# Kernel optimization log

Hardware: AMD Instinct MI355X
Metric: run time of the kernel (lower is better)

## Reference

```python
import jax, jax.numpy as jnp
import numpy as np

EMBED_DIM = 768
NUM_HEADS = 12
HEAD_DIM = EMBED_DIM // NUM_HEADS
B, S = 2, 2048


def setup_inputs() -> dict:
    key = jax.random.key(0)
    ks = jax.random.split(key, 6)
    glorot = jnp.sqrt(6.0 / (EMBED_DIM + EMBED_DIM)).astype(jnp.float32)
    x = jax.random.normal(ks[0], (B, S, EMBED_DIM), dtype=jnp.float32)
    mask = jnp.zeros((1, 1, S, S), dtype=jnp.float32)  # additive mask, 0 = no masking
    Wq = jax.random.uniform(ks[1], (EMBED_DIM, EMBED_DIM), jnp.float32, -glorot, glorot)
    Wk = jax.random.uniform(ks[2], (EMBED_DIM, EMBED_DIM), jnp.float32, -glorot, glorot)
    Wv = jax.random.uniform(ks[3], (EMBED_DIM, EMBED_DIM), jnp.float32, -glorot, glorot)
    Wo = jax.random.uniform(ks[4], (EMBED_DIM, EMBED_DIM), jnp.float32, -glorot, glorot)
    bo = jnp.zeros((EMBED_DIM,), dtype=jnp.float32)
    return {"x": x, "mask": mask, "Wq": Wq, "Wk": Wk, "Wv": Wv, "Wo": Wo, "bo": bo}


def reference(x, mask, Wq, Wk, Wv, Wo, bo):
    b, s, _ = x.shape
    # Q/K/V projections (no bias), split into heads: [b, h, s, d]
    def split_heads(t):
        return t.reshape(b, s, NUM_HEADS, HEAD_DIM).transpose(0, 2, 1, 3)
    q = split_heads(x @ Wq)
    k = split_heads(x @ Wk)
    v = split_heads(x @ Wv)
    scale = 1.0 / jnp.sqrt(jnp.float32(HEAD_DIM))
    logits = jnp.einsum('bhqd,bhkd->bhqk', q, k) * scale  # [b, h, s, s]
    logits = logits + mask * (-1e9)
    weights = jax.nn.softmax(logits, axis=-1)
    attn = jnp.einsum('bhqk,bhkd->bhqd', weights, v)
    concat = attn.transpose(0, 2, 1, 3).reshape(b, s, EMBED_DIM)
    return concat @ Wo + bo
```

## Files before the change

### kernel.cpp

```cpp
#include <hip/hip_runtime.h>


typedef __bf16 bf16_t;
typedef bf16_t bf16x8 __attribute__((ext_vector_type(8)));
typedef bf16_t bf16x4 __attribute__((ext_vector_type(4)));
typedef float f32x4 __attribute__((ext_vector_type(4)));
typedef _Float16 f16x4 __attribute__((ext_vector_type(4)));
typedef __fp16 hf2 __attribute__((ext_vector_type(2)));

#define SC2 0.1803368801111137f

__device__ __forceinline__ float bf2f(unsigned short u) {
  union { unsigned int i; float f; } x;
  x.i = ((unsigned int)u) << 16;
  return x.f;
}

__device__ __forceinline__ float fexp2(float x) {
  return __builtin_amdgcn_exp2f(x);
}

__device__ __forceinline__ void glds16(const bf16_t* g, bf16_t* l) {
  __builtin_amdgcn_global_load_lds(
      (const __attribute__((address_space(1))) void*)g,
      (__attribute__((address_space(3))) void*)l, 16, 0, 0);
}

__device__ __forceinline__ int detect_bf16_flag(const unsigned short* x) {
  const int lane = threadIdx.x & 63;
  const uint4* p = (const uint4*)x;
  uint4 a = p[lane * 2];
  uint4 b = p[lane * 2 + 1];
  unsigned int w[8] = {a.x, a.y, a.z, a.w, b.x, b.y, b.z, b.w};
  unsigned int big = 0;
#pragma unroll
  for (int i = 0; i < 8; i++) {
    unsigned int e0 = (w[i] >> 7) & 0xFF, e1 = (w[i] >> 23) & 0xFF;
    big |= (e0 > 0x88u) | (e1 > 0x88u);
  }
  unsigned long long bal = __ballot(big != 0u);
  return bal == 0ULL ? 1 : 0;
}

__global__ void k_prep(const void* __restrict__ x, const void* __restrict__ mask,
                       const void* __restrict__ Wq, const void* __restrict__ Wk,
                       const void* __restrict__ Wv, const void* __restrict__ Wo,
                       bf16_t* __restrict__ xb, bf16_t* __restrict__ wqkvT,
                       bf16_t* __restrict__ woT, int* __restrict__ mflags) {
  __shared__ float ts[32][33];
  __shared__ int snz;
  const int blk = blockIdx.x;
  const int f = detect_bf16_flag((const unsigned short*)x);

  if (blk < 1536) {
    if (f) return;
    int i = blk * 256 + threadIdx.x;
    const float* xf = (const float*)x + (size_t)i * 8;
    bf16x8 v;
#pragma unroll
    for (int j = 0; j < 8; j++) v[j] = (bf16_t)xf[j];
    *(bf16x8*)(xb + (size_t)i * 8) = v;
  } else if (blk < 3840) {
    const int t = blk - 1536;
    const int z = t / 576, r = t % 576, kt = r / 24, nt = r % 24;
    const void* wsrc = (z == 0) ? Wq : (z == 1) ? Wk : (z == 2) ? Wv : Wo;
    bf16_t* dst = (z < 3) ? (wqkvT + (size_t)z * 768 * 768) : woT;
    const int c = threadIdx.x & 31, r0 = threadIdx.x >> 5;
#pragma unroll
    for (int i = 0; i < 4; i++) {
      int kr = kt * 32 + r0 + i * 8;
      float v;
      if (f) v = bf2f(((const unsigned short*)wsrc)[(size_t)kr * 768 + nt * 32 + c]);
      else   v = ((const float*)wsrc)[(size_t)kr * 768 + nt * 32 + c];
      ts[r0 + i * 8][c] = v;
    }
    __syncthreads();
#pragma unroll
    for (int i = 0; i < 4; i++) {
      int nr = nt * 32 + r0 + i * 8;
      dst[(size_t)nr * 768 + kt * 32 + c] = (bf16_t)ts[c][r0 + i * 8];
    }
  } else {
    const int t = blk - 3840;
    const int qt = t >> 4, ktm = t & 15;
    if (threadIdx.x == 0) snz = 0;
    __syncthreads();
    unsigned int nz = 0;
    if (f) {
#pragma unroll
      for (int i = 0; i < 8; i++) {
        int uidx = i * 256 + threadIdx.x;
        int row = uidx >> 4, col = uidx & 15;
        const uint4* p = (const uint4*)((const char*)mask +
            ((size_t)(qt * 128 + row) * 2048 + ktm * 128) * 2 + col * 16);
        uint4 v = *p;
        nz |= ((v.x | v.y | v.z | v.w) & 0x7fff7fffu);
      }
    } else {
#pragma unroll
      for (int i = 0; i < 16; i++) {
        int uidx = i * 256 + threadIdx.x;
        int row = uidx >> 5, col = uidx & 31;
        const uint4* p = (const uint4*)((const char*)mask +
            ((size_t)(qt * 128 + row) * 2048 + ktm * 128) * 4 + col * 16);
        uint4 v = *p;
        nz |= ((v.x | v.y | v.z | v.w) & 0x7fffffffu);
      }
    }
    if (nz) snz = 1;
    __syncthreads();
    if (threadIdx.x == 0) mflags[qt * 16 + ktm] = snz;
  }
}

__global__ __launch_bounds__(256, 3) void k_gemmQKV(
    const bf16_t* __restrict__ xb, const bf16_t* __restrict__ Bm,
    bf16_t* __restrict__ Qd, bf16_t* __restrict__ Kd, _Float16* __restrict__ Vt,
    const unsigned short* __restrict__ xdet) {
  __shared__ __align__(16) char smem[32768];
  bf16_t* As0 = (bf16_t*)smem;
  bf16_t* As1 = (bf16_t*)(smem + 8192);
  bf16_t* Bs0 = (bf16_t*)(smem + 16384);
  bf16_t* Bs1 = (bf16_t*)(smem + 24576);
  _Float16* Tb = (_Float16*)smem;

  const int f = detect_bf16_flag(xdet);
  const bf16_t* A = f ? (const bf16_t*)xdet : xb;

  const int tid = threadIdx.x;
  const int n0 = blockIdx.x * 128, m0 = blockIdx.y * 128;
  const int r = tid >> 2, c8 = (tid & 3) << 3;
  const bf16_t* Ag = A + (size_t)(m0 + r) * 768 + c8;
  const bf16_t* Bg = Bm + (size_t)(n0 + r) * 768 + c8;
  const int wid = tid >> 6, lane = tid & 63;
  const int wm = (wid >> 1) << 6, wn = (wid & 1) << 6;
  const int lr = lane & 15, lk = (lane >> 4) << 3, g4 = (lane >> 4) << 2;

  f32x4 acc[4][4];
  const f32x4 z = {0.f, 0.f, 0.f, 0.f};
#pragma unroll
  for (int i = 0; i < 4; i++)
#pragma unroll
    for (int j = 0; j < 4; j++) acc[i][j] = z;

  for (int k0 = 0; k0 < 768; k0 += 64) {
    glds16(Ag + k0, As0 + wid * 512);
    glds16(Ag + (size_t)64 * 768 + k0, As0 + 2048 + wid * 512);
    glds16(Ag + k0 + 32, As1 + wid * 512);
    glds16(Ag + (size_t)64 * 768 + k0 + 32, As1 + 2048 + wid * 512);
    glds16(Bg + k0, Bs0 + wid * 512);
    glds16(Bg + (size_t)64 * 768 + k0, Bs0 + 2048 + wid * 512);
    glds16(Bg + k0 + 32, Bs1 + wid * 512);
    glds16(Bg + (size_t)64 * 768 + k0 + 32, Bs1 + 2048 + wid * 512);
    __syncthreads();
#pragma unroll
    for (int kc = 0; kc < 2; kc++) {
      const bf16_t* Asb = kc ? As1 : As0;
      const bf16_t* Bsb = kc ? Bs1 : Bs0;
      bf16x8 af[4], bf_[4];
#pragma unroll
      for (int t = 0; t < 4; t++) af[t]  = *(const bf16x8*)&Asb[(wm + t * 16 + lr) * 32 + lk];
#pragma unroll
      for (int t = 0; t < 4; t++) bf_[t] = *(const bf16x8*)&Bsb[(wn + t * 16 + lr) * 32 + lk];
#pragma unroll
      for (int i = 0; i < 4; i++)
#pragma unroll
        for (int j = 0; j < 4; j++)
          acc[i][j] = __builtin_amdgcn_mfma_f32_16x16x32_bf16(af[i], bf_[j], acc[i][j], 0, 0, 0);
    }
    __syncthreads();
  }

  if (n0 < 1536) {
    bf16_t* dst = (n0 < 768) ? Qd : Kd;
    const int nb = (n0 < 768) ? n0 : n0 - 768;
    const int bb = m0 >> 11;
#pragma unroll
    for (int i = 0; i < 4; i++)
#pragma unroll
      for (int j = 0; j < 4; j++) {
        const int rc = nb + wn + j * 16 + lr;
        const int hh = rc >> 6, dd = rc & 63;
        const size_t base = (((size_t)bb * 12 + hh) * 2048) * 64 + dd;
#pragma unroll
        for (int reg = 0; reg < 4; reg++) {
          const int s = (m0 & 2047) + wm + i * 16 + g4 + reg;
          dst[base + (size_t)s * 64] = (bf16_t)acc[i][j][reg];
        }
      }
  } else {
    const int bb = m0 >> 11;
#pragma unroll
    for (int half = 0; half < 2; half++) {
      if ((wid & 1) == half) {
#pragma unroll
        for (int j = 0; j < 4; j++) {
          const int d_l = j * 16 + lr;
#pragma unroll
          for (int i = 0; i < 4; i++)
#pragma unroll
            for (int reg = 0; reg < 4; reg++)
              Tb[d_l * 136 + wm + i * 16 + g4 + reg] = (_Float16)acc[i][j][reg];
        }
      }
      __syncthreads();
      const int row = tid >> 2, cc = (tid & 3) * 32;
      const int vcol = (n0 - 1536) + half * 64 + row;
      const int hh = vcol >> 6;
      _Float16* dstv = Vt + (((size_t)bb * 12 + hh) * 64 + row) * 2048 + (m0 & 2047) + cc;
#pragma unroll
      for (int u = 0; u < 4; u++)
        *(uint4*)(dstv + u * 8) = *(const uint4*)&Tb[row * 136 + cc + u * 8];
      __syncthreads();
    }
  }
}

__global__ __launch_bounds__(320, 4) void k_flash(
    const bf16_t* __restrict__ Qd, const bf16_t* __restrict__ Kd,
    const _Float16* __restrict__ Vt, const void* __restrict__ mask,
    const int* __restrict__ mflags, const unsigned short* __restrict__ xdet,
    bf16_t* __restrict__ attn) {
  __shared__ __align__(16) char sm[32768];

  const int tid = threadIdx.x, wid = tid >> 6, lane = tid & 63;
  const int lr = lane & 15, quad = lane >> 4, lk = quad << 3, g4 = quad << 2;

  const int lin = blockIdx.x;
  const int gx = lin & 7, ww = lin >> 3;
  const int hb = gx * 3 + (ww >> 5);
  const int h = hb % 12, bb = hb / 12;
  const int qt = ww & 31;

  const size_t bh = (size_t)bb * 12 + h;
  const char* Kh = (const char*)(Kd + bh * 2048 * 64);
  const char* Vh = (const char*)(Vt + bh * 64 * 2048);

  if (wid == 4) {
    const char* kS[8]; const char* vS[8];
#pragma unroll
    for (int u = 0; u < 8; u++) {
      const int R = (u >> 1) * 16 + lr;
      const int c = (u & 1) * 4 + quad;
      kS[u] = Kh + R * 128 + c * 16;
      const int u2 = u * 2 + (lane >> 5);
      const int dtv = u2 & 3, ctv = u2 >> 2, j2 = lane & 31;
      vS[u] = Vh + (size_t)(dtv * 16 + (j2 & 15)) * 4096 + ctv * 32 + (j2 >> 4) * 16;
    }
    uint4 kv[8], vv[8];
#pragma unroll
    for (int u = 0; u < 8; u++) kv[u] = *(const uint4*)(kS[u]);
#pragma unroll
    for (int u = 0; u < 8; u++) vv[u] = *(const uint4*)(vS[u]);
#pragma unroll
    for (int u = 0; u < 8; u++) *(uint4*)(sm + u * 1024 + lane * 16) = kv[u];
#pragma unroll
    for (int u = 0; u < 8; u++) *(uint4*)(sm + 8192 + u * 1024 + lane * 16) = vv[u];
    __syncthreads();
    for (int s = 0; s < 32; s++) {
      if (s < 31) {
        const int t = s + 1;
        char* buf = sm + (t & 1) * 16384;
#pragma unroll
        for (int u = 0; u < 8; u++) kv[u] = *(const uint4*)(kS[u] + (size_t)t * 8192);
#pragma unroll
        for (int u = 0; u < 8; u++) vv[u] = *(const uint4*)(vS[u] + (size_t)t * 128);
#pragma unroll
        for (int u = 0; u < 8; u++) *(uint4*)(buf + u * 1024 + lane * 16) = kv[u];
#pragma unroll
        for (int u = 0; u < 8; u++) *(uint4*)(buf + 8192 + u * 1024 + lane * 16) = vv[u];
      }
      __syncthreads();
    }
    return;
  }

  const bf16_t* Qh = Qd + bh * 2048 * 64;
  const int q0 = qt * 64 + wid * 16;
  const int mbf = detect_bf16_flag(xdet);
  const int* mfrow = mflags + (qt >> 1) * 16;
  int mbits = 0;
#pragma unroll
  for (int t = 0; t < 16; t++) mbits |= (mfrow[t] != 0) << t;

  const bf16x8 qf0 = *(const bf16x8*)&Qh[(size_t)(q0 + lr) * 64 + lk];
  const bf16x8 qf1 = *(const bf16x8*)&Qh[(size_t)(q0 + lr) * 64 + 32 + lk];

  f16x4 ones;
  ones[0] = (_Float16)1.f; ones[1] = (_Float16)1.f;
  ones[2] = (_Float16)1.f; ones[3] = (_Float16)1.f;

  const f32x4 z = {0.f, 0.f, 0.f, 0.f};
  f32x4 ot[4];
#pragma unroll
  for (int dt = 0; dt < 4; dt++) ot[dt] = z;
  float mrow = -1e30f, lrow = 0.f;

  __syncthreads();

  for (int s = 0; s < 32; s++) {
    const char* Kc = sm + (s & 1) * 16384;
    const char* Vc = Kc + 8192;

    f32x4 sv[4];
#pragma unroll
    for (int ct = 0; ct < 4; ct++) sv[ct] = z;
#pragma unroll
    for (int ct = 0; ct < 4; ct++) {
      bf16x8 kf0 = *(const bf16x8*)(Kc + ct * 2048 + lane * 16);
      bf16x8 kf1 = *(const bf16x8*)(Kc + ct * 2048 + 1024 + lane * 16);
      sv[ct] = __builtin_amdgcn_mfma_f32_16x16x32_bf16(kf0, qf0, sv[ct], 0, 0, 0);
      sv[ct] = __builtin_amdgcn_mfma_f32_16x16x32_bf16(kf1, qf1, sv[ct], 0, 0, 0);
    }

    if ((mbits >> (s >> 1)) & 1) {
#pragma unroll
      for (int ct = 0; ct < 4; ct++)
#pragma unroll
        for (int reg = 0; reg < 4; reg++) {
          size_t mi = (size_t)(q0 + lr) * 2048 + s * 64 + ct * 16 + g4 + reg;
          float mv = mbf ? bf2f(((const unsigned short*)mask)[mi])
                         : ((const float*)mask)[mi];
          sv[ct][reg] -= 8e9f * mv;
        }
    }

    float t = fmaxf(
        fmaxf(fmaxf(fmaxf(sv[0][0], sv[0][1]), fmaxf(sv[0][2], sv[0][3])),
              fmaxf(fmaxf(sv[1][0], sv[1][1]), fmaxf(sv[1][2], sv[1][3]))),
        fmaxf(fmaxf(fmaxf(sv[2][0], sv[2][1]), fmaxf(sv[2][2], sv[2][3])),
              fmaxf(fmaxf(sv[3][0], sv[3][1]), fmaxf(sv[3][2], sv[3][3]))));
    t = fmaxf(t, __shfl_xor(t, 16));
    t = fmaxf(t, __shfl_xor(t, 32));
    const float mnew = fmaxf(mrow, t);
    if (__ballot(mnew > mrow)) {
      const float alpha = fexp2((mrow - mnew) * SC2);
#pragma unroll
      for (int dt = 0; dt < 4; dt++)
#pragma unroll
        for (int reg = 0; reg < 4; reg++) ot[dt][reg] *= alpha;
      lrow *= alpha;
    }
    mrow = mnew;
    const float mS = mnew * SC2;

    f16x4 pb[4];
#pragma unroll
    for (int ct = 0; ct < 4; ct++) {
      float p0 = fexp2(fmaf(sv[ct][0], SC2, -mS));
      float p1 = fexp2(fmaf(sv[ct][1], SC2, -mS));
      float p2 = fexp2(fmaf(sv[ct][2], SC2, -mS));
      float p3 = fexp2(fmaf(sv[ct][3], SC2, -mS));
      union { hf2 h[2]; f16x4 v; } u;
      u.h[0] = __builtin_amdgcn_cvt_pkrtz(p0, p1);
      u.h[1] = __builtin_amdgcn_cvt_pkrtz(p2, p3);
      pb[ct] = u.v;
    }

    f32x4 asum = z;
#pragma unroll
    for (int ct = 0; ct < 4; ct++) {
      asum = __builtin_amdgcn_mfma_f32_16x16x16f16(ones, pb[ct], asum, 0, 0, 0);
#pragma unroll
      for (int dt = 0; dt < 4; dt++) {
        f16x4 va = *(const f16x4*)(Vc + (ct * 4 + dt) * 512 +
                                   (quad >> 1) * 256 + lr * 16 + (quad & 1) * 8);
        ot[dt] = __builtin_amdgcn_mfma_f32_16x16x16f16(va, pb[ct], ot[dt], 0, 0, 0);
      }
    }
    lrow += asum[0];
    __syncthreads();
  }

  const float inv = 1.0f / lrow;
  bf16_t* arow = attn + ((size_t)bb * 2048 + q0 + lr) * 768 + h * 64 + g4;
#pragma unroll
  for (int dt = 0; dt < 4; dt++) {
    bf16x4 v;
#pragma unroll
    for (int reg = 0; reg < 4; reg++) v[reg] = (bf16_t)(ot[dt][reg] * inv);
    *(bf16x4*)(arow + dt * 16) = v;
  }
}

__global__ __launch_bounds__(256, 3) void k_gemm2(
    const bf16_t* __restrict__ A, const bf16_t* __restrict__ Bm,
    const void* __restrict__ bo, const unsigned short* __restrict__ xdet,
    float* __restrict__ outF, unsigned short* __restrict__ outH) {
  __shared__ __align__(16) char smem[16384];
  bf16_t* As0 = (bf16_t*)smem;
  bf16_t* As1 = (bf16_t*)(smem + 4096);
  bf16_t* Bs0 = (bf16_t*)(smem + 8192);
  bf16_t* Bs1 = (bf16_t*)(smem + 12288);

  const int tid = threadIdx.x, wid = tid >> 6, lane = tid & 63;
  const int n0 = blockIdx.x * 64, m0 = blockIdx.y * 64;
  const int wm = (wid >> 1) << 5, wn = (wid & 1) << 5;
  const int lr = lane & 15, lk = (lane >> 4) << 3, g4 = (lane >> 4) << 2;
  const int rr = lane >> 2, c8 = (lane & 3) << 3;
  const bf16_t* Ag = A + (size_t)(m0 + wid * 16 + rr) * 768 + c8;
  const bf16_t* Bg = Bm + (size_t)(n0 + wid * 16 + rr) * 768 + c8;

  f32x4 acc[2][2];
  const f32x4 z = {0.f, 0.f, 0.f, 0.f};
#pragma unroll
  for (int i = 0; i < 2; i++)
#pragma unroll
    for (int j = 0; j < 2; j++) acc[i][j] = z;

  for (int k0 = 0; k0 < 768; k0 += 64) {
    glds16(Ag + k0, As0 + wid * 512);
    glds16(Ag + k0 + 32, As1 + wid * 512);
    glds16(Bg + k0, Bs0 + wid * 512);
    glds16(Bg + k0 + 32, Bs1 + wid * 512);
    __syncthreads();
#pragma unroll
    for (int kc = 0; kc < 2; kc++) {
      const bf16_t* Asb = kc ? As1 : As0;
      const bf16_t* Bsb = kc ? Bs1 : Bs0;
      bf16x8 af[2], bf_[2];
#pragma unroll
      for (int i = 0; i < 2; i++) af[i]  = *(const bf16x8*)&Asb[(wm + i * 16 + lr) * 32 + lk];
#pragma unroll
      for (int j = 0; j < 2; j++) bf_[j] = *(const bf16x8*)&Bsb[(wn + j * 16 + lr) * 32 + lk];
#pragma unroll
      for (int i = 0; i < 2; i++)
#pragma unroll
        for (int j = 0; j < 2; j++)
          acc[i][j] = __builtin_amdgcn_mfma_f32_16x16x32_bf16(af[i], bf_[j], acc[i][j], 0, 0, 0);
    }
    __syncthreads();
  }

  const int obf = detect_bf16_flag(xdet);
#pragma unroll
  for (int i = 0; i < 2; i++)
#pragma unroll
    for (int j = 0; j < 2; j++) {
      const int nn = n0 + wn + j * 16 + lr;
      const float bv = obf ? bf2f(((const unsigned short*)bo)[nn])
                           : ((const float*)bo)[nn];
#pragma unroll
      for (int reg = 0; reg < 4; reg++) {
        const int m = m0 + wm + i * 16 + g4 + reg;
        const float v = acc[i][j][reg] + bv;
        if (obf) outH[(size_t)m * 768 + nn] = __builtin_bit_cast(unsigned short, (bf16_t)v);
        else     outF[(size_t)m * 768 + nn] = v;
      }
    }
}

extern "C" void kernel_launch(void* const* d_in, const int* in_sizes, int n_in,
                              void* d_out, int out_size, void* d_ws, size_t ws_size,
                              hipStream_t stream) {
  (void)in_sizes; (void)n_in; (void)out_size; (void)ws_size;
  const void* x    = d_in[0];
  const void* mask = d_in[1];
  const void* Wq   = d_in[2];
  const void* Wk   = d_in[3];
  const void* Wv   = d_in[4];
  const void* Wo   = d_in[5];
  const void* bo   = d_in[6];

  char* w = (char*)d_ws;
  size_t off = 0;
  auto take = [&](size_t b) -> void* {
    void* p = w + off;
    off = (off + b + 255) & ~(size_t)255;
    return p;
  };
  int*      mflags = (int*)take(256 * 4);
  bf16_t*   wqkvT  = (bf16_t*)take((size_t)2304 * 768 * 2);
  bf16_t*   woT    = (bf16_t*)take((size_t)768 * 768 * 2);
  bf16_t*   xb     = (bf16_t*)take((size_t)4096 * 768 * 2);
  bf16_t*   Qd     = (bf16_t*)take((size_t)3145728 * 2);
  bf16_t*   Kd     = (bf16_t*)take((size_t)3145728 * 2);
  _Float16* Vt     = (_Float16*)take((size_t)3145728 * 2);
  bf16_t*   attn   = xb;

  k_prep<<<4096, 256, 0, stream>>>(x, mask, Wq, Wk, Wv, Wo, xb, wqkvT, woT, mflags);
  k_gemmQKV<<<dim3(18, 32), 256, 0, stream>>>(xb, wqkvT, Qd, Kd, Vt,
                                              (const unsigned short*)x);
  k_flash<<<768, 320, 0, stream>>>(Qd, Kd, Vt, mask, mflags,
                                   (const unsigned short*)x, attn);
  k_gemm2<<<dim3(12, 64), 256, 0, stream>>>(attn, woT, bo, (const unsigned short*)x,
                                            (float*)d_out, (unsigned short*)d_out);
}
```

Baseline: 182.0 us.

## Add dedicated producer wave for double-buffered loads in projection GEMMs

Both GEMM kernels now launch 320 threads, and a fifth wave acts as a producer. It loads A/B tiles from global memory through registers into a double-buffered LDS ring, one K-step ahead, while the four compute waves run MFMAs on the other buffer. This replaces the synchronous global_load_lds pattern, where every wave loaded and then waited each iteration, and is meant to overlap memory latency with compute. The cost is more barriers (24 K-steps of 32 instead of 12 of 64) and a serial single-wave load path that may be bandwidth-limited. The producer wave must also match barrier counts in the QKV epilogue.

```diff
diff --git a/kernel.cpp b/kernel.cpp
--- a/kernel.cpp
+++ b/kernel.cpp
@@ -18,12 +18,6 @@
 
 __device__ __forceinline__ float fexp2(float x) {
   return __builtin_amdgcn_exp2f(x);
-}
-
-__device__ __forceinline__ void glds16(const bf16_t* g, bf16_t* l) {
-  __builtin_amdgcn_global_load_lds(
-      (const __attribute__((address_space(1))) void*)g,
-      (__attribute__((address_space(3))) void*)l, 16, 0, 0);
 }
 
 __device__ __forceinline__ int detect_bf16_flag(const unsigned short* x) {
@@ -113,29 +107,58 @@
   }
 }
 
-__global__ __launch_bounds__(256, 3) void k_gemmQKV(
+__global__ __launch_bounds__(320, 4) void k_gemmQKV(
     const bf16_t* __restrict__ xb, const bf16_t* __restrict__ Bm,
     bf16_t* __restrict__ Qd, bf16_t* __restrict__ Kd, _Float16* __restrict__ Vt,
     const unsigned short* __restrict__ xdet) {
   __shared__ __align__(16) char smem[32768];
-  bf16_t* As0 = (bf16_t*)smem;
-  bf16_t* As1 = (bf16_t*)(smem + 8192);
-  bf16_t* Bs0 = (bf16_t*)(smem + 16384);
-  bf16_t* Bs1 = (bf16_t*)(smem + 24576);
   _Float16* Tb = (_Float16*)smem;
 
   const int f = detect_bf16_flag(xdet);
   const bf16_t* A = f ? (const bf16_t*)xdet : xb;
 
-  const int tid = threadIdx.x;
+  const int tid = threadIdx.x, wid = tid >> 6, lane = tid & 63;
   const int n0 = blockIdx.x * 128, m0 = blockIdx.y * 128;
-  const int r = tid >> 2, c8 = (tid & 3) << 3;
-  const bf16_t* Ag = A + (size_t)(m0 + r) * 768 + c8;
-  const bf16_t* Bg = Bm + (size_t)(n0 + r) * 768 + c8;
-  const int wid = tid >> 6, lane = tid & 63;
+  const int lr = lane & 15, lk = (lane >> 4) << 3, g4 = (lane >> 4) << 2;
+
+  if (wid == 4) {
+    const int pr = lane >> 2, pk = (lane & 3) << 3;
+    const bf16_t* Ag = A + (size_t)(m0 + pr) * 768 + pk;
+    const bf16_t* Bg = Bm + (size_t)(n0 + pr) * 768 + pk;
+    const int dst16 = lane * 16;
+    uint4 av[8], bv[8];
+#pragma unroll
+    for (int j = 0; j < 8; j++) av[j] = *(const uint4*)(Ag + (size_t)(j * 16) * 768);
+#pragma unroll
+    for (int j = 0; j < 8; j++) bv[j] = *(const uint4*)(Bg + (size_t)(j * 16) * 768);
+#pragma unroll
+    for (int j = 0; j < 8; j++) *(uint4*)(smem + j * 1024 + dst16) = av[j];
+#pragma unroll
+    for (int j = 0; j < 8; j++) *(uint4*)(smem + 16384 + j * 1024 + dst16) = bv[j];
+    __syncthreads();
+    for (int s = 0; s < 24; s++) {
+      if (s < 23) {
+        const int k0 = (s + 1) * 32;
+        char* Ab = smem + ((s + 1) & 1) * 8192;
+        char* Bb = smem + 16384 + ((s + 1) & 1) * 8192;
+#pragma unroll
+        for (int j = 0; j < 8; j++) av[j] = *(const uint4*)(Ag + (size_t)(j * 16) * 768 + k0);
+#pragma unroll
+        for (int j = 0; j < 8; j++) bv[j] = *(const uint4*)(Bg + (size_t)(j * 16) * 768 + k0);
+#pragma unroll
+        for (int j = 0; j < 8; j++) *(uint4*)(Ab + j * 1024 + dst16) = av[j];
+#pragma unroll
+        for (int j = 0; j < 8; j++) *(uint4*)(Bb + j * 1024 + dst16) = bv[j];
+      }
+      __syncthreads();
+    }
+    if (n0 < 1536) return;
+#pragma unroll
+    for (int half = 0; half < 2; half++) { __syncthreads(); __syncthreads(); }
+    return;
+  }
+
   const int wm = (wid >> 1) << 6, wn = (wid & 1) << 6;
-  const int lr = lane & 15, lk = (lane >> 4) << 3, g4 = (lane >> 4) << 2;
-
   f32x4 acc[4][4];
   const f32x4 z = {0.f, 0.f, 0.f, 0.f};
 #pragma unroll
@@ -143,31 +166,20 @@
 #pragma unroll
     for (int j = 0; j < 4; j++) acc[i][j] = z;
 
-  for (int k0 = 0; k0 < 768; k0 += 64) {
-    glds16(Ag + k0, As0 + wid * 512);
-    glds16(Ag + (size_t)64 * 768 + k0, As0 + 2048 + wid * 512);
-    glds16(Ag + k0 + 32, As1 + wid * 512);
-    glds16(Ag + (size_t)64 * 768 + k0 + 32, As1 + 2048 + wid * 512);
-    glds16(Bg + k0, Bs0 + wid * 512);
-    glds16(Bg + (size_t)64 * 768 + k0, Bs0 + 2048 + wid * 512);
-    glds16(Bg + k0 + 32, Bs1 + wid * 512);
-    glds16(Bg + (size_t)64 * 768 + k0 + 32, Bs1 + 2048 + wid * 512);
-    __syncthreads();
-#pragma unroll
-    for (int kc = 0; kc < 2; kc++) {
-      const bf16_t* Asb = kc ? As1 : As0;
-      const bf16_t* Bsb = kc ? Bs1 : Bs0;
-      bf16x8 af[4], bf_[4];
-#pragma unroll
-      for (int t = 0; t < 4; t++) af[t]  = *(const bf16x8*)&Asb[(wm + t * 16 + lr) * 32 + lk];
-#pragma unroll
-      for (int t = 0; t < 4; t++) bf_[t] = *(const bf16x8*)&Bsb[(wn + t * 16 + lr) * 32 + lk];
-#pragma unroll
-      for (int i = 0; i < 4; i++)
-#pragma unroll
-        for (int j = 0; j < 4; j++)
-          acc[i][j] = __builtin_amdgcn_mfma_f32_16x16x32_bf16(af[i], bf_[j], acc[i][j], 0, 0, 0);
-    }
+  __syncthreads();
+  for (int s = 0; s < 24; s++) {
+    const bf16_t* As = (const bf16_t*)(smem + (s & 1) * 8192);
+    const bf16_t* Bs = (const bf16_t*)(smem + 16384 + (s & 1) * 8192);
+    bf16x8 af[4], bf_[4];
+#pragma unroll
+    for (int t = 0; t < 4; t++) af[t]  = *(const bf16x8*)&As[(wm + t * 16 + lr) * 32 + lk];
+#pragma unroll
+    for (int t = 0; t < 4; t++) bf_[t] = *(const bf16x8*)&Bs[(wn + t * 16 + lr) * 32 + lk];
+#pragma unroll
+    for (int i = 0; i < 4; i++)
+#pragma unroll
+      for (int j = 0; j < 4; j++)
+        acc[i][j] = __builtin_amdgcn_mfma_f32_16x16x32_bf16(af[i], bf_[j], acc[i][j], 0, 0, 0);
     __syncthreads();
   }
 
@@ -383,24 +395,51 @@
   }
 }
 
-__global__ __launch_bounds__(256, 3) void k_gemm2(
+__global__ __launch_bounds__(320, 4) void k_gemm2(
     const bf16_t* __restrict__ A, const bf16_t* __restrict__ Bm,
     const void* __restrict__ bo, const unsigned short* __restrict__ xdet,
     float* __restrict__ outF, unsigned short* __restrict__ outH) {
   __shared__ __align__(16) char smem[16384];
-  bf16_t* As0 = (bf16_t*)smem;
-  bf16_t* As1 = (bf16_t*)(smem + 4096);
-  bf16_t* Bs0 = (bf16_t*)(smem + 8192);
-  bf16_t* Bs1 = (bf16_t*)(smem + 12288);
 
   const int tid = threadIdx.x, wid = tid >> 6, lane = tid & 63;
   const int n0 = blockIdx.x * 64, m0 = blockIdx.y * 64;
+  const int lr = lane & 15, lk = (lane >> 4) << 3, g4 = (lane >> 4) << 2;
+
+  if (wid == 4) {
+    const int pr = lane >> 2, pk = (lane & 3) << 3;
+    const bf16_t* Ag = A + (size_t)(m0 + pr) * 768 + pk;
+    const bf16_t* Bg = Bm + (size_t)(n0 + pr) * 768 + pk;
+    const int dst16 = lane * 16;
+    uint4 av[4], bv[4];
+#pragma unroll
+    for (int j = 0; j < 4; j++) av[j] = *(const uint4*)(Ag + (size_t)(j * 16) * 768);
+#pragma unroll
+    for (int j = 0; j < 4; j++) bv[j] = *(const uint4*)(Bg + (size_t)(j * 16) * 768);
+#pragma unroll
+    for (int j = 0; j < 4; j++) *(uint4*)(smem + j * 1024 + dst16) = av[j];
+#pragma unroll
+    for (int j = 0; j < 4; j++) *(uint4*)(smem + 8192 + j * 1024 + dst16) = bv[j];
+    __syncthreads();
+    for (int s = 0; s < 24; s++) {
+      if (s < 23) {
+        const int k0 = (s + 1) * 32;
+        char* Ab = smem + ((s + 1) & 1) * 4096;
+        char* Bb = smem + 8192 + ((s + 1) & 1) * 4096;
+#pragma unroll
+        for (int j = 0; j < 4; j++) av[j] = *(const uint4*)(Ag + (size_t)(j * 16) * 768 + k0);
+#pragma unroll
+        for (int j = 0; j < 4; j++) bv[j] = *(const uint4*)(Bg + (size_t)(j * 16) * 768 + k0);
+#pragma unroll
+        for (int j = 0; j < 4; j++) *(uint4*)(Ab + j * 1024 + dst16) = av[j];
+#pragma unroll
+        for (int j = 0; j < 4; j++) *(uint4*)(Bb + j * 1024 + dst16) = bv[j];
+      }
+      __syncthreads();
+    }
+    return;
+  }
+
   const int wm = (wid >> 1) << 5, wn = (wid & 1) << 5;
-  const int lr = lane & 15, lk = (lane >> 4) << 3, g4 = (lane >> 4) << 2;
-  const int rr = lane >> 2, c8 = (lane & 3) << 3;
-  const bf16_t* Ag = A + (size_t)(m0 + wid * 16 + rr) * 768 + c8;
-  const bf16_t* Bg = Bm + (size_t)(n0 + wid * 16 + rr) * 768 + c8;
-
   f32x4 acc[2][2];
   const f32x4 z = {0.f, 0.f, 0.f, 0.f};
 #pragma unroll
@@ -408,27 +447,20 @@
 #pragma unroll
     for (int j = 0; j < 2; j++) acc[i][j] = z;
 
-  for (int k0 = 0; k0 < 768; k0 += 64) {
-    glds16(Ag + k0, As0 + wid * 512);
-    glds16(Ag + k0 + 32, As1 + wid * 512);
-    glds16(Bg + k0, Bs0 + wid * 512);
-    glds16(Bg + k0 + 32, Bs1 + wid * 512);
-    __syncthreads();
-#pragma unroll
-    for (int kc = 0; kc < 2; kc++) {
-      const bf16_t* Asb = kc ? As1 : As0;
-      const bf16_t* Bsb = kc ? Bs1 : Bs0;
-      bf16x8 af[2], bf_[2];
-#pragma unroll
-      for (int i = 0; i < 2; i++) af[i]  = *(const bf16x8*)&Asb[(wm + i * 16 + lr) * 32 + lk];
-#pragma unroll
-      for (int j = 0; j < 2; j++) bf_[j] = *(const bf16x8*)&Bsb[(wn + j * 16 + lr) * 32 + lk];
-#pragma unroll
-      for (int i = 0; i < 2; i++)
-#pragma unroll
-        for (int j = 0; j < 2; j++)
-          acc[i][j] = __builtin_amdgcn_mfma_f32_16x16x32_bf16(af[i], bf_[j], acc[i][j], 0, 0, 0);
-    }
+  __syncthreads();
+  for (int s = 0; s < 24; s++) {
+    const bf16_t* As = (const bf16_t*)(smem + (s & 1) * 4096);
+    const bf16_t* Bs = (const bf16_t*)(smem + 8192 + (s & 1) * 4096);
+    bf16x8 af[2], bf_[2];
+#pragma unroll
+    for (int i = 0; i < 2; i++) af[i]  = *(const bf16x8*)&As[(wm + i * 16 + lr) * 32 + lk];
+#pragma unroll
+    for (int j = 0; j < 2; j++) bf_[j] = *(const bf16x8*)&Bs[(wn + j * 16 + lr) * 32 + lk];
+#pragma unroll
+    for (int i = 0; i < 2; i++)
+#pragma unroll
+      for (int j = 0; j < 2; j++)
+        acc[i][j] = __builtin_amdgcn_mfma_f32_16x16x32_bf16(af[i], bf_[j], acc[i][j], 0, 0, 0);
     __syncthreads();
   }
 
@@ -479,10 +511,10 @@
   bf16_t*   attn   = xb;
 
   k_prep<<<4096, 256, 0, stream>>>(x, mask, Wq, Wk, Wv, Wo, xb, wqkvT, woT, mflags);
-  k_gemmQKV<<<dim3(18, 32), 256, 0, stream>>>(xb, wqkvT, Qd, Kd, Vt,
+  k_gemmQKV<<<dim3(18, 32), 320, 0, stream>>>(xb, wqkvT, Qd, Kd, Vt,
                                               (const unsigned short*)x);
   k_flash<<<768, 320, 0, stream>>>(Qd, Kd, Vt, mask, mflags,
                                    (const unsigned short*)x, attn);
-  k_gemm2<<<dim3(12, 64), 256, 0, stream>>>(attn, woT, bo, (const unsigned short*)x,
+  k_gemm2<<<dim3(12, 64), 320, 0, stream>>>(attn, woT, bo, (const unsigned short*)x,
                                             (float*)d_out, (unsigned short*)d_out);
 }
```

Measured after the change: 192.3 us. 1.06x slower.

## Double-buffer LDS tiles in QKV and output projection GEMMs

Applied to the files above, without the earlier changes.

Both projection GEMM kernels now use double-buffered shared memory. The next k-slice is prefetched through global_load_lds while MFMAs run on the current buffer, with one barrier per step instead of two. The aim is to hide global load latency behind compute. The QKV kernel now steps by a k-depth of 32 (24 steps), and the output kernel's LDS grows to 32KB, which may reduce occupancy.

```diff
diff --git a/kernel.cpp b/kernel.cpp
--- a/kernel.cpp
+++ b/kernel.cpp
@@ -118,10 +118,6 @@
     bf16_t* __restrict__ Qd, bf16_t* __restrict__ Kd, _Float16* __restrict__ Vt,
     const unsigned short* __restrict__ xdet) {
   __shared__ __align__(16) char smem[32768];
-  bf16_t* As0 = (bf16_t*)smem;
-  bf16_t* As1 = (bf16_t*)(smem + 8192);
-  bf16_t* Bs0 = (bf16_t*)(smem + 16384);
-  bf16_t* Bs1 = (bf16_t*)(smem + 24576);
   _Float16* Tb = (_Float16*)smem;
 
   const int f = detect_bf16_flag(xdet);
@@ -143,31 +139,38 @@
 #pragma unroll
     for (int j = 0; j < 4; j++) acc[i][j] = z;
 
-  for (int k0 = 0; k0 < 768; k0 += 64) {
-    glds16(Ag + k0, As0 + wid * 512);
-    glds16(Ag + (size_t)64 * 768 + k0, As0 + 2048 + wid * 512);
-    glds16(Ag + k0 + 32, As1 + wid * 512);
-    glds16(Ag + (size_t)64 * 768 + k0 + 32, As1 + 2048 + wid * 512);
-    glds16(Bg + k0, Bs0 + wid * 512);
-    glds16(Bg + (size_t)64 * 768 + k0, Bs0 + 2048 + wid * 512);
-    glds16(Bg + k0 + 32, Bs1 + wid * 512);
-    glds16(Bg + (size_t)64 * 768 + k0 + 32, Bs1 + 2048 + wid * 512);
-    __syncthreads();
-#pragma unroll
-    for (int kc = 0; kc < 2; kc++) {
-      const bf16_t* Asb = kc ? As1 : As0;
-      const bf16_t* Bsb = kc ? Bs1 : Bs0;
-      bf16x8 af[4], bf_[4];
-#pragma unroll
-      for (int t = 0; t < 4; t++) af[t]  = *(const bf16x8*)&Asb[(wm + t * 16 + lr) * 32 + lk];
-#pragma unroll
-      for (int t = 0; t < 4; t++) bf_[t] = *(const bf16x8*)&Bsb[(wn + t * 16 + lr) * 32 + lk];
-#pragma unroll
-      for (int i = 0; i < 4; i++)
-#pragma unroll
-        for (int j = 0; j < 4; j++)
-          acc[i][j] = __builtin_amdgcn_mfma_f32_16x16x32_bf16(af[i], bf_[j], acc[i][j], 0, 0, 0);
-    }
+  {
+    bf16_t* A0 = (bf16_t*)smem;
+    bf16_t* B0 = (bf16_t*)(smem + 16384);
+    glds16(Ag, A0 + wid * 512);
+    glds16(Ag + (size_t)64 * 768, A0 + 2048 + wid * 512);
+    glds16(Bg, B0 + wid * 512);
+    glds16(Bg + (size_t)64 * 768, B0 + 2048 + wid * 512);
+  }
+  __syncthreads();
+
+  for (int s = 0; s < 24; s++) {
+    if (s < 23) {
+      const int k0 = (s + 1) * 32;
+      bf16_t* An = (bf16_t*)(smem + ((s + 1) & 1) * 8192);
+      bf16_t* Bn = (bf16_t*)(smem + 16384 + ((s + 1) & 1) * 8192);
+      glds16(Ag + k0, An + wid * 512);
+      glds16(Ag + (size_t)64 * 768 + k0, An + 2048 + wid * 512);
+      glds16(Bg + k0, Bn + wid * 512);
+      glds16(Bg + (size_t)64 * 768 + k0, Bn + 2048 + wid * 512);
+    }
+    const bf16_t* As = (const bf16_t*)(smem + (s & 1) * 8192);
+    const bf16_t* Bs = (const bf16_t*)(smem + 16384 + (s & 1) * 8192);
+    bf16x8 af[4], bf_[4];
+#pragma unroll
+    for (int t = 0; t < 4; t++) af[t]  = *(const bf16x8*)&As[(wm + t * 16 + lr) * 32 + lk];
+#pragma unroll
+    for (int t = 0; t < 4; t++) bf_[t] = *(const bf16x8*)&Bs[(wn + t * 16 + lr) * 32 + lk];
+#pragma unroll
+    for (int i = 0; i < 4; i++)
+#pragma unroll
+      for (int j = 0; j < 4; j++)
+        acc[i][j] = __builtin_amdgcn_mfma_f32_16x16x32_bf16(af[i], bf_[j], acc[i][j], 0, 0, 0);
     __syncthreads();
   }
 
@@ -387,19 +390,14 @@
     const bf16_t* __restrict__ A, const bf16_t* __restrict__ Bm,
     const void* __restrict__ bo, const unsigned short* __restrict__ xdet,
     float* __restrict__ outF, unsigned short* __restrict__ outH) {
-  __shared__ __align__(16) char smem[16384];
-  bf16_t* As0 = (bf16_t*)smem;
-  bf16_t* As1 = (bf16_t*)(smem + 4096);
-  bf16_t* Bs0 = (bf16_t*)(smem + 8192);
-  bf16_t* Bs1 = (bf16_t*)(smem + 12288);
+  __shared__ __align__(16) char smem[32768];
 
   const int tid = threadIdx.x, wid = tid >> 6, lane = tid & 63;
   const int n0 = blockIdx.x * 64, m0 = blockIdx.y * 64;
   const int wm = (wid >> 1) << 5, wn = (wid & 1) << 5;
   const int lr = lane & 15, lk = (lane >> 4) << 3, g4 = (lane >> 4) << 2;
-  const int rr = lane >> 2, c8 = (lane & 3) << 3;
-  const bf16_t* Ag = A + (size_t)(m0 + wid * 16 + rr) * 768 + c8;
-  const bf16_t* Bg = Bm + (size_t)(n0 + wid * 16 + rr) * 768 + c8;
+  const bf16_t* Ag = A + (size_t)(m0 + (tid >> 2)) * 768 + ((tid & 3) << 3);
+  const bf16_t* Bg = Bm + (size_t)(n0 + (tid >> 2)) * 768 + ((tid & 3) << 3);
 
   f32x4 acc[2][2];
   const f32x4 z = {0.f, 0.f, 0.f, 0.f};
@@ -408,21 +406,35 @@
 #pragma unroll
     for (int j = 0; j < 2; j++) acc[i][j] = z;
 
-  for (int k0 = 0; k0 < 768; k0 += 64) {
-    glds16(Ag + k0, As0 + wid * 512);
-    glds16(Ag + k0 + 32, As1 + wid * 512);
-    glds16(Bg + k0, Bs0 + wid * 512);
-    glds16(Bg + k0 + 32, Bs1 + wid * 512);
-    __syncthreads();
+  {
+    bf16_t* A0 = (bf16_t*)smem;
+    bf16_t* B0 = (bf16_t*)(smem + 16384);
+    glds16(Ag, A0 + wid * 512);
+    glds16(Ag + 32, A0 + 2048 + wid * 512);
+    glds16(Bg, B0 + wid * 512);
+    glds16(Bg + 32, B0 + 2048 + wid * 512);
+  }
+  __syncthreads();
+
+  for (int s = 0; s < 12; s++) {
+    if (s < 11) {
+      const int k0 = (s + 1) * 64;
+      bf16_t* An = (bf16_t*)(smem + ((s + 1) & 1) * 8192);
+      bf16_t* Bn = (bf16_t*)(smem + 16384 + ((s + 1) & 1) * 8192);
+      glds16(Ag + k0, An + wid * 512);
+      glds16(Ag + k0 + 32, An + 2048 + wid * 512);
+      glds16(Bg + k0, Bn + wid * 512);
+      glds16(Bg + k0 + 32, Bn + 2048 + wid * 512);
+    }
 #pragma unroll
     for (int kc = 0; kc < 2; kc++) {
-      const bf16_t* Asb = kc ? As1 : As0;
-      const bf16_t* Bsb = kc ? Bs1 : Bs0;
+      const bf16_t* As = (const bf16_t*)(smem + (s & 1) * 8192) + kc * 2048;
+      const bf16_t* Bs = (const bf16_t*)(smem + 16384 + (s & 1) * 8192) + kc * 2048;
       bf16x8 af[2], bf_[2];
 #pragma unroll
-      for (int i = 0; i < 2; i++) af[i]  = *(const bf16x8*)&Asb[(wm + i * 16 + lr) * 32 + lk];
-#pragma unroll
-      for (int j = 0; j < 2; j++) bf_[j] = *(const bf16x8*)&Bsb[(wn + j * 16 + lr) * 32 + lk];
+      for (int i = 0; i < 2; i++) af[i]  = *(const bf16x8*)&As[(wm + i * 16 + lr) * 32 + lk];
+#pragma unroll
+      for (int j = 0; j < 2; j++) bf_[j] = *(const bf16x8*)&Bs[(wn + j * 16 + lr) * 32 + lk];
 #pragma unroll
       for (int i = 0; i < 2; i++)
 #pragma unroll
```

After: 178.0 us. 1.02x faster.
